# Kernel optimization log

Hardware: AMD Instinct MI355X
Metric: run time of the kernel (lower is better)

## Reference

```python
import jax, jax.numpy as jnp
import numpy as np

B = 4096
IN_F = 4096
OUT_F = 4096
IN_Q = IN_F // 4
OUT_Q = OUT_F // 4


def setup_inputs() -> dict:
    key = jax.random.key(0)
    ks = jax.random.split(key, 9)
    scale = 1.0 / np.sqrt(IN_Q)
    inp = {"x": jax.random.normal(ks[0], (B, IN_F), dtype=jnp.float32)}
    for i, name in enumerate(["rr", "ri", "rj", "rk"]):
        inp[f"W_{name}"] = jax.random.uniform(ks[1 + i], (OUT_Q, IN_Q), dtype=jnp.float32, minval=-scale, maxval=scale)
        inp[f"b_{name}"] = jax.random.uniform(ks[5 + i], (OUT_Q,), dtype=jnp.float32, minval=-scale, maxval=scale)
    return inp


def reference(x, W_rr, W_ri, W_rj, W_rk, b_rr, b_ri, b_rj, b_rk):
    b = x.shape[0]
    # split into quaternion components: chunks c in {r,i,j,k}
    xs = x.reshape(b, 4, IN_Q)                       # [B, 4, IN_Q]
    W = jnp.stack([W_rr, W_ri, W_rj, W_rk])          # [4(lin), OUT_Q, IN_Q]
    bias = jnp.stack([b_rr, b_ri, b_rj, b_rk])       # [4(lin), OUT_Q]
    # all 16 linear applications in one batched GEMM: Y[b,c,q,:] = lin_q(x_c)
    Y = jnp.einsum('bci,qoi->bcqo', xs, W) + bias    # [B, 4, 4, OUT_Q]
    out_r = Y[:, 0, 0] - Y[:, 1, 1] - Y[:, 2, 2] - Y[:, 3, 3]
    out_i = Y[:, 0, 1] + Y[:, 1, 0] + Y[:, 2, 3] - Y[:, 3, 2]
    out_j = Y[:, 0, 2] - Y[:, 1, 3] + Y[:, 2, 0] + Y[:, 3, 1]
    out_k = Y[:, 0, 3] + Y[:, 1, 2] - Y[:, 2, 1] + Y[:, 3, 0]
    out = jnp.stack([out_r, out_i, out_j, out_k], axis=1)  # [B, 4, OUT_Q]
    return out.reshape(b, -1)                        # [B, OUT_F]
```

## Files before the change

kernel.cpp:

```cpp
#include <hip/hip_runtime.h>
#include <cstdint>
#include <cstddef>

#define MDIM 4096
#define NDIM 4096
#define KDIM 4096

typedef _Float16 half8   __attribute__((ext_vector_type(8)));
typedef float    floatx4 __attribute__((ext_vector_type(4)));

__device__ __constant__ int   d_qtab[16] = {0,1,2,3,  1,0,3,2,  2,3,0,1,  3,2,1,0};
__device__ __constant__ float d_stab[16] = {1.f,-1.f,-1.f,-1.f,
                                            1.f, 1.f, 1.f,-1.f,
                                            1.f,-1.f, 1.f, 1.f,
                                            1.f, 1.f,-1.f, 1.f};

__global__ void prepass_kernel(const float* __restrict__ x,
                               const float* __restrict__ W0, const float* __restrict__ W1,
                               const float* __restrict__ W2, const float* __restrict__ W3,
                               _Float16* __restrict__ xh, _Float16* __restrict__ Wh) {
    int b = blockIdx.x;
    if (b < 8192) {
        int idx = b * 256 + threadIdx.x;
        const float4* src = (const float4*)x + (size_t)idx * 2;
        float4 a = src[0], v = src[1];
        half8 h = {(_Float16)a.x, (_Float16)a.y, (_Float16)a.z, (_Float16)a.w,
                   (_Float16)v.x, (_Float16)v.y, (_Float16)v.z, (_Float16)v.w};
        ((half8*)xh)[idx] = h;
    } else {
        int idx = (b - 8192) * 256 + threadIdx.x;
        int e = idx << 3;
        int m = e >> 20;
        int off = e & ((1 << 20) - 1);
        const float* Ws[4] = {W0, W1, W2, W3};
        const float* src = Ws[m] + off;
        float4 a = *(const float4*)src;
        float4 v = *(const float4*)(src + 4);
        half8 h = {(_Float16)a.x, (_Float16)a.y, (_Float16)a.z, (_Float16)a.w,
                   (_Float16)v.x, (_Float16)v.y, (_Float16)v.z, (_Float16)v.w};
        *(half8*)(Wh + ((size_t)m << 20) + off) = h;
    }
}


__device__ __forceinline__ void gload_lds16(const _Float16* g, _Float16* l) {
    __builtin_amdgcn_global_load_lds(
        (const __attribute__((address_space(1))) unsigned int*)g,
        (__attribute__((address_space(3))) unsigned int*)l,
        16, 0, 0);
}

__global__ __launch_bounds__(256, 2) void gemm_kernel(
        const _Float16* __restrict__ A,
        const _Float16* __restrict__ Wh,
        const float* __restrict__ b0, const float* __restrict__ b1,
        const float* __restrict__ b2, const float* __restrict__ b3,
        float* __restrict__ C) {
    __shared__ _Float16 As[256 * 64];
    __shared__ _Float16 Bs[128 * 64];

    const int tid  = threadIdx.x;
    const int lane = tid & 63;
    const int wave = tid >> 6;
    const int wm = (wave & 1) * 128;
    const int wn = (wave >> 1) * 64;

    const int g = blockIdx.x;
    const int bm = g >> 5;
    const int bn = g & 31;
    const int m0 = bm * 256;
    const int n0 = bn * 128;
    const int comp = n0 >> 10;

    const int lrow = tid >> 3;
    const int gch  = (tid & 7) ^ (lrow & 7);
    const _Float16* Ag0 = A + (size_t)(m0 + lrow) * KDIM + gch * 8;
    const int brow0 = (n0 & 1023) + lrow;

    floatx4 acc[8][4];
#pragma unroll
    for (int i = 0; i < 8; i++)
#pragma unroll
        for (int j = 0; j < 4; j++)
            acc[i][j] = (floatx4){0.f, 0.f, 0.f, 0.f};

    const int fr = lane & 15;
    const int qf = lane >> 4;
    const int fsw = fr & 7;
    const int slot_s0 = (((0) + qf) ^ fsw) * 8;
    const int slot_s1 = (((4) + qf) ^ fsw) * 8;

    for (int c = 0; c < 4; c++) {
        const int t = comp * 4 + c;
        const _Float16* Bg0 = Wh + ((size_t)d_qtab[t] << 20)
                                 + (size_t)brow0 * 1024 + gch * 8;
        const _Float16* Ag  = Ag0 + c * 1024;
        const _Float16 s = (_Float16)d_stab[t];
        half8 sv = {s, s, s, s, s, s, s, s};

        for (int kk = 0; kk < 1024; kk += 64) {
#pragma unroll
            for (int r = 0; r < 8; r++)
                gload_lds16(Ag + kk + (size_t)r * 32 * KDIM, As + r * 2048 + tid * 8);
#pragma unroll
            for (int r = 0; r < 4; r++)
                gload_lds16(Bg0 + kk + (size_t)r * 32 * 1024, Bs + r * 2048 + tid * 8);
            __syncthreads();

#pragma unroll
            for (int s2 = 0; s2 < 2; s2++) {
                const int slot = s2 ? slot_s1 : slot_s0;
                half8 af[8], bf[4];
#pragma unroll
                for (int j = 0; j < 4; j++)
                    bf[j] = *(const half8*)(Bs + (wn + j * 16 + fr) * 64 + slot) * sv;
#pragma unroll
                for (int i = 0; i < 8; i++)
                    af[i] = *(const half8*)(As + (wm + i * 16 + fr) * 64 + slot);
#pragma unroll
                for (int i = 0; i < 8; i++)
#pragma unroll
                    for (int j = 0; j < 4; j++)
                        acc[i][j] = __builtin_amdgcn_mfma_f32_16x16x32_f16(
                            af[i], bf[j], acc[i][j], 0, 0, 0);
            }

            __syncthreads();
        }
    }

    const int col   = lane & 15;
    const int rquad = (lane >> 4) * 4;
    const float* bs[4] = {b0, b1, b2, b3};
#pragma unroll
    for (int j = 0; j < 4; j++) {
        const int gn = n0 + wn + j * 16 + col;
        const int o  = gn & 1023;
        float bv = 0.f;
#pragma unroll
        for (int c = 0; c < 4; c++)
            bv += d_stab[comp * 4 + c] * bs[d_qtab[comp * 4 + c]][o];
#pragma unroll
        for (int i = 0; i < 8; i++) {
            const int gmb = m0 + wm + i * 16 + rquad;
#pragma unroll
            for (int r = 0; r < 4; r++)
                C[(size_t)(gmb + r) * NDIM + gn] = acc[i][j][r] + bv;
        }
    }
}

__global__ void fallback_kernel(const float* __restrict__ x,
                                const float* __restrict__ W0, const float* __restrict__ W1,
                                const float* __restrict__ W2, const float* __restrict__ W3,
                                const float* __restrict__ b0, const float* __restrict__ b1,
                                const float* __restrict__ b2, const float* __restrict__ b3,
                                float* __restrict__ out) {
    int idx = blockIdx.x * 256 + threadIdx.x;
    int m = idx >> 12, n = idx & 4095;
    int comp = n >> 10, o = n & 1023;
    const float* Ws[4] = {W0, W1, W2, W3};
    const float* bs[4] = {b0, b1, b2, b3};
    float acc = 0.f;
    for (int c = 0; c < 4; c++) {
        int t = comp * 4 + c;
        const float* wr = Ws[d_qtab[t]] + (size_t)o * 1024;
        const float* xr = x + (size_t)m * 4096 + c * 1024;
        float s = d_stab[t];
        float dot = 0.f;
        for (int i = 0; i < 1024; i += 4) {
            float4 wv = *(const float4*)(wr + i);
            float4 xv = *(const float4*)(xr + i);
            dot += wv.x * xv.x + wv.y * xv.y + wv.z * xv.z + wv.w * xv.w;
        }
        acc += s * dot + s * bs[d_qtab[t]][o];
    }
    out[idx] = acc;
}

extern "C" void kernel_launch(void* const* d_in, const int* in_sizes, int n_in,
                              void* d_out, int out_size, void* d_ws, size_t ws_size,
                              hipStream_t stream) {
    const float* x = (const float*)d_in[0];
    const float* W[4];
    const float* b[4];
    int wi = 0, bi = 0;
    for (int i = 1; i < n_in && i < 9; i++) {
        if (in_sizes[i] > 4096) { if (wi < 4) W[wi++] = (const float*)d_in[i]; }
        else                    { if (bi < 4) b[bi++] = (const float*)d_in[i]; }
    }
    float* out = (float*)d_out;

    const size_t xh_elems = (size_t)MDIM * KDIM;
    const size_t wh_elems = (size_t)4 * 1024 * 1024;
    const size_t needed = (xh_elems + wh_elems) * 2;

    if (ws_size < needed) {
        fallback_kernel<<<(MDIM * NDIM) / 256, 256, 0, stream>>>(
            x, W[0], W[1], W[2], W[3], b[0], b[1], b[2], b[3], out);
        return;
    }

    _Float16* xh = (_Float16*)d_ws;
    _Float16* Wh = xh + xh_elems;

    prepass_kernel<<<8192 + 2048, 256, 0, stream>>>(x, W[0], W[1], W[2], W[3], xh, Wh);
    gemm_kernel<<<(MDIM / 256) * (NDIM / 128), 256, 0, stream>>>(
        xh, Wh, b[0], b[1], b[2], b[3], out);
}
```

Baseline: 269.2 us.

## Restructure GEMM into double-buffered 256x256 tile pipeline with interleaved loads

The GEMM moves from a 256x128 tile on 4 waves to a 256x256 tile on 8 waves. It uses double-buffered LDS and software pipelining, so global-to-LDS loads for upcoming k-steps are issued between MFMA phases with explicit vmcnt/lgkmcnt waits and barriers. The quaternion sign handling moves to a per-segment negate of B plus a final flip, and the block index is remapped for locality. This aims to hide memory latency and cut per-iteration barrier stalls, at the cost of 128KB LDS per block and delicate manual wait counts.

```diff
diff --git a/kernel.cpp b/kernel.cpp
--- a/kernel.cpp
+++ b/kernel.cpp
@@ -50,32 +50,90 @@
         16, 0, 0);
 }
 
-__global__ __launch_bounds__(256, 2) void gemm_kernel(
+#define BAR __builtin_amdgcn_s_barrier()
+#define WAITLGKM do { asm volatile("s_waitcnt lgkmcnt(0)" ::: "memory"); \
+                      __builtin_amdgcn_sched_barrier(0); } while (0)
+#define WAITVM(N) asm volatile("s_waitcnt vmcnt(" #N ")" ::: "memory")
+
+#define STA(g, tt, buf) { \
+    const _Float16* _s = Abase + (size_t)((g) * 64) * KDIM + (tt) * 64; \
+    _Float16* _d = AsSt + (buf) * 16384 + (g) * 8192; \
+    gload_lds16(_s, _d); \
+    gload_lds16(_s + (size_t)128 * KDIM, _d + 4096); }
+
+#define STB(h, tt, buf) { \
+    const int _sg = (tt) >> 4; \
+    const _Float16* _s = Bbase + ((size_t)(comp ^ _sg) << 20) \
+                       + (size_t)((h) * 128) * 1024 + ((tt) & 15) * 64; \
+    _Float16* _d = BsSt + (buf) * 16384 + (h) * 8192; \
+    gload_lds16(_s, _d); \
+    gload_lds16(_s + 64 * 1024, _d + 4096); }
+
+#define RDA(g, SL) { \
+    const _Float16* _p = Acur + (g) * 8192 + arow + (SL); \
+    af[0] = *(const half8*)(_p); \
+    af[1] = *(const half8*)(_p + 1024); \
+    af[2] = *(const half8*)(_p + 2048); \
+    af[3] = *(const half8*)(_p + 3072); }
+
+#define RDB(BQ, SL) { \
+    const _Float16* _p = Bcur + bnh * 8192 + brow + (SL); \
+    BQ[0] = *(const half8*)(_p); \
+    BQ[1] = *(const half8*)(_p + 1024); \
+    BQ[2] = *(const half8*)(_p + 2048); \
+    BQ[3] = *(const half8*)(_p + 3072); \
+    if (bneg) { BQ[0] = -BQ[0]; BQ[1] = -BQ[1]; BQ[2] = -BQ[2]; BQ[3] = -BQ[3]; } }
+
+#define MFMA16(IB, BQ) \
+    _Pragma("unroll") \
+    for (int _i = 0; _i < 4; _i++) \
+      _Pragma("unroll") \
+      for (int _j = 0; _j < 4; _j++) \
+        acc[(IB) + _i][_j] = __builtin_amdgcn_mfma_f32_16x16x32_f16( \
+            af[_i], BQ[_j], acc[(IB) + _i][_j], 0, 0, 0);
+
+__global__ __launch_bounds__(512, 2) void gemm_kernel(
         const _Float16* __restrict__ A,
         const _Float16* __restrict__ Wh,
         const float* __restrict__ b0, const float* __restrict__ b1,
         const float* __restrict__ b2, const float* __restrict__ b3,
         float* __restrict__ C) {
-    __shared__ _Float16 As[256 * 64];
-    __shared__ _Float16 Bs[128 * 64];
+    __shared__ _Float16 lds[65536];
+    _Float16* As = lds;
+    _Float16* Bs = lds + 32768;
 
     const int tid  = threadIdx.x;
     const int lane = tid & 63;
     const int wave = tid >> 6;
-    const int wm = (wave & 1) * 128;
-    const int wn = (wave >> 1) * 64;
-
-    const int g = blockIdx.x;
-    const int bm = g >> 5;
-    const int bn = g & 31;
-    const int m0 = bm * 256;
-    const int n0 = bn * 128;
-    const int comp = n0 >> 10;
+    const int wmh  = wave >> 2;
+    const int wn   = (wave & 3) * 64;
+    const int bnh  = wn >> 7;
+    const int broff = (wn & 64) * 64;
+
+    const int wg = ((blockIdx.x & 7) << 5) | (blockIdx.x >> 3);
+    const int bm = wg >> 4, bn = wg & 15;
+    const int m0 = bm << 8;
+    const int n0 = bn << 8;
+    const int comp = bn >> 2;
+    const int n0q  = n0 & 1023;
 
     const int lrow = tid >> 3;
     const int gch  = (tid & 7) ^ (lrow & 7);
-    const _Float16* Ag0 = A + (size_t)(m0 + lrow) * KDIM + gch * 8;
-    const int brow0 = (n0 & 1023) + lrow;
+    const _Float16* Abase = A  + (size_t)(m0  + lrow) * KDIM + gch * 8;
+    const _Float16* Bbase = Wh + (size_t)(n0q + lrow) * 1024 + gch * 8;
+    _Float16* AsSt = As + tid * 8;
+    _Float16* BsSt = Bs + tid * 8;
+
+    const int fr  = lane & 15;
+    const int qf  = lane >> 4;
+    const int fsw = fr & 7;
+    const int sl0 = ((0 + qf) ^ fsw) * 8;
+    const int sl1 = ((4 + qf) ^ fsw) * 8;
+    const int arow = wmh * 4096 + fr * 64;
+    const int brow = broff + fr * 64;
+
+    const int negseg = (comp == 0) ? 0 : (comp == 1) ? 3 : (comp == 2) ? 1 : 2;
+    const float flip = (comp == 0) ? -1.f : 1.f;
 
     floatx4 acc[8][4];
 #pragma unroll
@@ -84,54 +142,61 @@
         for (int j = 0; j < 4; j++)
             acc[i][j] = (floatx4){0.f, 0.f, 0.f, 0.f};
 
-    const int fr = lane & 15;
-    const int qf = lane >> 4;
-    const int fsw = fr & 7;
-    const int slot_s0 = (((0) + qf) ^ fsw) * 8;
-    const int slot_s1 = (((4) + qf) ^ fsw) * 8;
-
-    for (int c = 0; c < 4; c++) {
-        const int t = comp * 4 + c;
-        const _Float16* Bg0 = Wh + ((size_t)d_qtab[t] << 20)
-                                 + (size_t)brow0 * 1024 + gch * 8;
-        const _Float16* Ag  = Ag0 + c * 1024;
-        const _Float16 s = (_Float16)d_stab[t];
-        half8 sv = {s, s, s, s, s, s, s, s};
-
-        for (int kk = 0; kk < 1024; kk += 64) {
-#pragma unroll
-            for (int r = 0; r < 8; r++)
-                gload_lds16(Ag + kk + (size_t)r * 32 * KDIM, As + r * 2048 + tid * 8);
-#pragma unroll
-            for (int r = 0; r < 4; r++)
-                gload_lds16(Bg0 + kk + (size_t)r * 32 * 1024, Bs + r * 2048 + tid * 8);
-            __syncthreads();
-
-#pragma unroll
-            for (int s2 = 0; s2 < 2; s2++) {
-                const int slot = s2 ? slot_s1 : slot_s0;
-                half8 af[8], bf[4];
-#pragma unroll
-                for (int j = 0; j < 4; j++)
-                    bf[j] = *(const half8*)(Bs + (wn + j * 16 + fr) * 64 + slot) * sv;
-#pragma unroll
-                for (int i = 0; i < 8; i++)
-                    af[i] = *(const half8*)(As + (wm + i * 16 + fr) * 64 + slot);
-#pragma unroll
-                for (int i = 0; i < 8; i++)
-#pragma unroll
-                    for (int j = 0; j < 4; j++)
-                        acc[i][j] = __builtin_amdgcn_mfma_f32_16x16x32_f16(
-                            af[i], bf[j], acc[i][j], 0, 0, 0);
-            }
-
-            __syncthreads();
-        }
-    }
+    STA(0, 0, 0); STB(0, 0, 0); STB(1, 0, 0); STA(1, 0, 0);
+    STA(0, 1, 1); STB(0, 1, 1);
+    WAITVM(6);
+    BAR;
+
+    for (int tt = 0; tt < 64; ++tt) {
+        const int cur = tt & 1, nxt = cur ^ 1;
+        const bool bneg = ((tt >> 4) == negseg);
+        const _Float16* Acur = As + cur * 16384;
+        const _Float16* Bcur = Bs + cur * 16384;
+        const int t1 = (tt >= 63) ? 63 : tt + 1;
+        const int t2 = (tt >= 62) ? 63 : tt + 2;
+        half8 af[4], bf0[4], bf1[4];
+
+        RDA(0, sl0); RDB(bf0, sl0);
+        STB(1, t1, nxt);
+        BAR; WAITLGKM;
+        __builtin_amdgcn_s_setprio(1);
+        MFMA16(0, bf0);
+        __builtin_amdgcn_s_setprio(0);
+        BAR;
+
+        RDA(0, sl1); RDB(bf1, sl1);
+        STA(1, t1, nxt);
+        BAR; WAITLGKM;
+        __builtin_amdgcn_s_setprio(1);
+        MFMA16(0, bf1);
+        __builtin_amdgcn_s_setprio(0);
+        WAITVM(8);
+        BAR;
+
+        RDA(1, sl0);
+        STA(0, t2, cur);
+        BAR; WAITLGKM;
+        __builtin_amdgcn_s_setprio(1);
+        MFMA16(4, bf0);
+        __builtin_amdgcn_s_setprio(0);
+        BAR;
+
+        RDA(1, sl1);
+        STB(0, t2, cur);
+        BAR; WAITLGKM;
+        __builtin_amdgcn_s_setprio(1);
+        MFMA16(4, bf1);
+        __builtin_amdgcn_s_setprio(0);
+        WAITVM(6);
+        BAR;
+    }
+
+    WAITVM(0);
 
     const int col   = lane & 15;
     const int rquad = (lane >> 4) * 4;
-    const float* bs[4] = {b0, b1, b2, b3};
+    const int wm    = wmh * 128;
+    const float* bsp[4] = {b0, b1, b2, b3};
 #pragma unroll
     for (int j = 0; j < 4; j++) {
         const int gn = n0 + wn + j * 16 + col;
@@ -139,13 +204,13 @@
         float bv = 0.f;
 #pragma unroll
         for (int c = 0; c < 4; c++)
-            bv += d_stab[comp * 4 + c] * bs[d_qtab[comp * 4 + c]][o];
+            bv += d_stab[comp * 4 + c] * bsp[comp ^ c][o];
 #pragma unroll
         for (int i = 0; i < 8; i++) {
             const int gmb = m0 + wm + i * 16 + rquad;
 #pragma unroll
             for (int r = 0; r < 4; r++)
-                C[(size_t)(gmb + r) * NDIM + gn] = acc[i][j][r] + bv;
+                C[(size_t)(gmb + r) * NDIM + gn] = flip * acc[i][j][r] + bv;
         }
     }
 }
@@ -205,6 +270,6 @@
     _Float16* Wh = xh + xh_elems;
 
     prepass_kernel<<<8192 + 2048, 256, 0, stream>>>(x, W[0], W[1], W[2], W[3], xh, Wh);
-    gemm_kernel<<<(MDIM / 256) * (NDIM / 128), 256, 0, stream>>>(
+    gemm_kernel<<<(MDIM / 256) * (NDIM / 256), 512, 0, stream>>>(
         xh, Wh, b[0], b[1], b[2], b[3], out);
 }
```

After: 259.2 us. 3.7% less time.
